# Performance work log

Measured on AMD Instinct MI355X. Metric: run time of the kernel, lower is better.

## Reference

```python
import jax, jax.numpy as jnp
import numpy as np

B, C, T = 8, 1025, 3000


def setup_inputs() -> dict:
    key = jax.random.key(0)
    k1, k2 = jax.random.split(key)
    x_real = jax.random.normal(k1, (B, C, T), dtype=jnp.float32)
    x_imag = jax.random.normal(k2, (B, C, T), dtype=jnp.float32)
    return {"x_real": x_real, "x_imag": x_imag}


def reference(x_real, x_imag):
    # coherent_polar: magnitude + min-max-normalized unwrapped phase, cat on channel dim
    magnitude = jnp.sqrt(x_real * x_real + x_imag * x_imag)  # torch.abs(complex)
    phase = jnp.arctan2(x_imag, x_real)                      # torch.angle

    pi = jnp.float32(np.pi)
    two_pi = jnp.float32(2.0 * np.pi)

    phase_diff = phase[:, :, 1:] - phase[:, :, :-1]          # [B, C, T-1]
    # per-step correction: +2pi where diff < -pi, -2pi where diff > pi
    steps = jnp.where(phase_diff < -pi, two_pi, jnp.float32(0.0)) \
          + jnp.where(phase_diff > pi, -two_pi, jnp.float32(0.0))
    # the original sequential loop is an inclusive prefix-sum of the steps
    correction = jnp.concatenate(
        [jnp.zeros_like(phase[:, :, :1]), jnp.cumsum(steps, axis=2)], axis=2
    )  # [B, C, T]

    unwrapped = phase + correction
    phase_min = jnp.min(unwrapped, axis=2, keepdims=True)
    phase_max = jnp.max(unwrapped, axis=2, keepdims=True)
    phase_norm = (unwrapped - phase_min) / (phase_max - phase_min + 1e-8)

    return jnp.concatenate([magnitude, phase_norm], axis=1)  # [B, 2C, T]
```

## Files before the change

### kernel.cpp

```cpp
#include <hip/hip_runtime.h>

namespace {
constexpr int kB = 8;
constexpr int kC = 1025;
constexpr int kRows = kB * kC;
constexpr int kT = 3000;
constexpr int kThreads = 256;
constexpr int kWaves = kThreads / 64;
constexpr int kSeg = kThreads * 4;
constexpr int kNSeg = 3;
constexpr int kGridB = 2050;
constexpr int kRowsPer = 4;
constexpr float kPi = 3.14159265358979323846f;
constexpr float kTwoPi = 6.28318530717958647692f;
constexpr float kPiO2 = 1.57079632679489661923f;
}

typedef float v4f __attribute__((ext_vector_type(4)));
typedef float v2f __attribute__((ext_vector_type(2)));

__device__ __forceinline__ void sync_lds() {
  asm volatile("s_waitcnt lgkmcnt(0)" ::: "memory");
  __builtin_amdgcn_s_barrier();
  asm volatile("" ::: "memory");
}

__device__ __forceinline__ v2f atan_core2(v2f t) {
  const v2f s = t * t;
  v2f p = v2f{0.00282363896258175373f, 0.00282363896258175373f};
  p = p * s + v2f{-0.0159569028764963150f, -0.0159569028764963150f};
  p = p * s + v2f{0.0425049886107444763f, 0.0425049886107444763f};
  p = p * s + v2f{-0.0748900920152664185f, -0.0748900920152664185f};
  p = p * s + v2f{0.106347933411598206f, 0.106347933411598206f};
  p = p * s + v2f{-0.142027363181114197f, -0.142027363181114197f};
  p = p * s + v2f{0.199926957488059998f, 0.199926957488059998f};
  p = p * s + v2f{-0.333331018686294556f, -0.333331018686294556f};
  return (p * s) * t + t;
}

__device__ __forceinline__ void fast_atan2_4(const v4f y4, const v4f x4,
                                             float out[4]) {
  float t[4], ax[4], ay[4];
  const float xs[4] = {x4.x, x4.y, x4.z, x4.w};
  const float ys[4] = {y4.x, y4.y, y4.z, y4.w};
#pragma unroll
  for (int k = 0; k < 4; ++k) {
    ax[k] = __builtin_fabsf(xs[k]);
    ay[k] = __builtin_fabsf(ys[k]);
    const float mx = fmaxf(ax[k], ay[k]);
    const float mn = fminf(ax[k], ay[k]);
    float tt = mn * __builtin_amdgcn_rcpf(mx);
    if (mx == 0.0f) tt = 0.0f;
    t[k] = tt;
  }
  const v2f a01 = atan_core2(v2f{t[0], t[1]});
  const v2f a23 = atan_core2(v2f{t[2], t[3]});
  const float av[4] = {a01.x, a01.y, a23.x, a23.y};
#pragma unroll
  for (int k = 0; k < 4; ++k) {
    float a = av[k];
    a = (ay[k] > ax[k]) ? (kPiO2 - a) : a;
    a = (xs[k] < 0.0f) ? (kPi - a) : a;
    out[k] = copysignf(a, ys[k]);
  }
}

__device__ __forceinline__ void load_row(const float* __restrict__ re,
                                         const float* __restrict__ im,
                                         int tid, v4f r4[kNSeg], v4f i4[kNSeg]) {
#pragma unroll
  for (int s = 0; s < kNSeg; ++s) {
    const int off = s * kSeg + tid * 4;
    if (s < 2 || off < kT) {
      r4[s] = *reinterpret_cast<const v4f*>(re + off);
      i4[s] = *reinterpret_cast<const v4f*>(im + off);
    }
  }
}

__global__ __launch_bounds__(kThreads, 4) void coherent_polar_kernel(
    const float* __restrict__ xr, const float* __restrict__ xi,
    float* __restrict__ out) {
  __shared__ float s_last[kNSeg][kThreads];
  __shared__ float s_wsum[kWaves][kNSeg];
  __shared__ float s_wmin[kWaves][kNSeg];
  __shared__ float s_wmax[kWaves][kNSeg];

  const int bid = blockIdx.x;
  const int tid = threadIdx.x;
  const int lane = tid & 63;
  const int wave = tid >> 6;
  const bool act2 = tid * 4 + 2 * kSeg < kT;

  v4f r4[kNSeg], i4[kNSeg], r4n[kNSeg], i4n[kNSeg];
  load_row(xr + (size_t)bid * kT, xi + (size_t)bid * kT, tid, r4, i4);

#pragma unroll 1
  for (int r = 0; r < kRowsPer; ++r) {
    const int row = bid + r * kGridB;
    const int b = row / kC;
    const int c = row - b * kC;
    float* mag_out = out + ((size_t)b * (2 * kC) + c) * kT;
    float* ph_out  = out + ((size_t)b * (2 * kC) + kC + c) * kT;

    float ph[kNSeg][4];
#pragma unroll
    for (int s = 0; s < kNSeg; ++s) {
      if (s < 2 || act2) {
        v4f m4;
        m4.x = __builtin_amdgcn_sqrtf(fmaf(r4[s].x, r4[s].x, i4[s].x * i4[s].x));
        m4.y = __builtin_amdgcn_sqrtf(fmaf(r4[s].y, r4[s].y, i4[s].y * i4[s].y));
        m4.z = __builtin_amdgcn_sqrtf(fmaf(r4[s].z, r4[s].z, i4[s].z * i4[s].z));
        m4.w = __builtin_amdgcn_sqrtf(fmaf(r4[s].w, r4[s].w, i4[s].w * i4[s].w));
        __builtin_nontemporal_store(m4, reinterpret_cast<v4f*>(mag_out + s * kSeg + tid * 4));
        fast_atan2_4(i4[s], r4[s], ph[s]);
      }
    }

    if (r + 1 < kRowsPer) {
      const int nrow = row + kGridB;
      load_row(xr + (size_t)nrow * kT, xi + (size_t)nrow * kT, tid, r4n, i4n);
    }

#pragma unroll
    for (int s = 0; s < kNSeg; ++s)
      s_last[s][tid] = (s < 2 || act2) ? ph[s][3] : 0.0f;
    sync_lds();
    float prevph[kNSeg];
#pragma unroll
    for (int s = 0; s < kNSeg; ++s) {
      if (tid > 0)       prevph[s] = s_last[s][tid - 1];
      else if (s > 0)    prevph[s] = s_last[s - 1][kThreads - 1];
      else               prevph[s] = ph[0][0];
    }

    float T[kNSeg];
#pragma unroll
    for (int s = 0; s < kNSeg; ++s) {
      float run = 0.0f;
      if (s < 2 || act2) {
        float p = prevph[s];
#pragma unroll
        for (int k = 0; k < 4; ++k) {
          const float cur = ph[s][k];
          const float d = cur - p;
          p = cur;
          float step = 0.0f;
          if (d < -kPi) step = kTwoPi;
          else if (d > kPi) step = -kTwoPi;
          run += step;
          ph[s][k] = cur + run;
        }
      }
      T[s] = (s < 2 || act2) ? run : 0.0f;
    }

    float inc[kNSeg] = {T[0], T[1], T[2]};
#pragma unroll
    for (int d = 1; d < 64; d <<= 1) {
#pragma unroll
      for (int s = 0; s < kNSeg; ++s) {
        const float n = __shfl_up(inc[s], d);
        if (lane >= d) inc[s] += n;
      }
    }
    float excl[kNSeg];
#pragma unroll
    for (int s = 0; s < kNSeg; ++s) excl[s] = inc[s] - T[s];

    float mn[kNSeg], mx[kNSeg];
#pragma unroll
    for (int s = 0; s < kNSeg; ++s) {
      mn[s] = __builtin_inff();
      mx[s] = -__builtin_inff();
      if (s < 2 || act2) {
#pragma unroll
        for (int k = 0; k < 4; ++k) {
          const float u = ph[s][k] + excl[s];
          mn[s] = fminf(mn[s], u);
          mx[s] = fmaxf(mx[s], u);
        }
      }
    }
#pragma unroll
    for (int m = 32; m >= 1; m >>= 1) {
#pragma unroll
      for (int s = 0; s < kNSeg; ++s) {
        mn[s] = fminf(mn[s], __shfl_xor(mn[s], m));
        mx[s] = fmaxf(mx[s], __shfl_xor(mx[s], m));
      }
    }
    if (lane == 63) {
#pragma unroll
      for (int s = 0; s < kNSeg; ++s) s_wsum[wave][s] = inc[s];
    }
    if (lane == 0) {
#pragma unroll
      for (int s = 0; s < kNSeg; ++s) { s_wmin[wave][s] = mn[s]; s_wmax[wave][s] = mx[s]; }
    }
    sync_lds();

    float wavePref[kWaves][kNSeg];
    float blockTot[kNSeg];
#pragma unroll
    for (int s = 0; s < kNSeg; ++s) {
      float acc = 0.0f;
#pragma unroll
      for (int w = 0; w < kWaves; ++w) { wavePref[w][s] = acc; acc += s_wsum[w][s]; }
      blockTot[s] = acc;
    }
    float segBase[kNSeg];
    segBase[0] = 0.0f;
    segBase[1] = blockTot[0];
    segBase[2] = blockTot[0] + blockTot[1];

    float gmn = __builtin_inff();
    float gmx = -__builtin_inff();
#pragma unroll
    for (int w = 0; w < kWaves; ++w) {
#pragma unroll
      for (int s = 0; s < kNSeg; ++s) {
        const float off = segBase[s] + wavePref[w][s];
        gmn = fminf(gmn, s_wmin[w][s] + off);
        gmx = fmaxf(gmx, s_wmax[w][s] + off);
      }
    }
    const float inv = 1.0f / (gmx - gmn + 1e-8f);

#pragma unroll
    for (int s = 0; s < kNSeg; ++s) {
      if (s < 2 || act2) {
        const float base = segBase[s] + wavePref[wave][s] + excl[s] - gmn;
        v4f o;
        o.x = (ph[s][0] + base) * inv;
        o.y = (ph[s][1] + base) * inv;
        o.z = (ph[s][2] + base) * inv;
        o.w = (ph[s][3] + base) * inv;
        __builtin_nontemporal_store(o, reinterpret_cast<v4f*>(ph_out + s * kSeg + tid * 4));
      }
    }

    if (r + 1 < kRowsPer) {
#pragma unroll
      for (int s = 0; s < kNSeg; ++s) { r4[s] = r4n[s]; i4[s] = i4n[s]; }
    }
  }
}

extern "C" void kernel_launch(void* const* d_in, const int* in_sizes, int n_in,
                              void* d_out, int out_size, void* d_ws, size_t ws_size,
                              hipStream_t stream) {
  const float* xr = (const float*)d_in[0];
  const float* xi = (const float*)d_in[1];
  float* out = (float*)d_out;
  coherent_polar_kernel<<<dim3(kGridB), dim3(kThreads), 0, stream>>>(xr, xi, out);
}
```

Measured before the change: 70.18 us.

## Give each wave a contiguous segment and cut block scan to one barrier

Each wave now owns a contiguous 768-element chunk of the row, so the inter-thread phase boundary is handled with shuffles and readlane instead of an LDS exchange and barrier. Wrap counts are packed as three 10-bit integers into one word, giving a single integer shuffle scan instead of three float scans. The min/max reduction uses DPP row operations, and cross-wave combination uses a double-buffered LDS slot with one barrier per row. The next-row prefetch is also issued before compute. This relies on the packed counts not overflowing their 10-bit fields, and it adds register pressure from the early prefetch.

```diff
diff --git a/kernel.cpp b/kernel.cpp
--- a/kernel.cpp
+++ b/kernel.cpp
@@ -3,17 +3,17 @@
 namespace {
 constexpr int kB = 8;
 constexpr int kC = 1025;
-constexpr int kRows = kB * kC;
 constexpr int kT = 3000;
 constexpr int kThreads = 256;
-constexpr int kWaves = kThreads / 64;
-constexpr int kSeg = kThreads * 4;
-constexpr int kNSeg = 3;
+constexpr int kWSeg = 768;
+constexpr int kSub = 256;
+constexpr int kNS = 3;
 constexpr int kGridB = 2050;
 constexpr int kRowsPer = 4;
 constexpr float kPi = 3.14159265358979323846f;
 constexpr float kTwoPi = 6.28318530717958647692f;
 constexpr float kPiO2 = 1.57079632679489661923f;
+constexpr float kInv2Pi = 0.15915494309189533577f;
 }
 
 typedef float v4f __attribute__((ext_vector_type(4)));
@@ -23,6 +23,28 @@
   asm volatile("s_waitcnt lgkmcnt(0)" ::: "memory");
   __builtin_amdgcn_s_barrier();
   asm volatile("" ::: "memory");
+}
+
+__device__ __forceinline__ float rdlane_f(float v, int l) {
+  return __builtin_bit_cast(
+      float, __builtin_amdgcn_readlane(__builtin_bit_cast(int, v), l));
+}
+
+template <int kCtrl>
+__device__ __forceinline__ float dpp_f(float v) {
+  return __builtin_bit_cast(
+      float, __builtin_amdgcn_update_dpp(__builtin_bit_cast(int, v),
+                                         __builtin_bit_cast(int, v), kCtrl,
+                                         0xF, 0xF, false));
+}
+
+__device__ __forceinline__ void wave_minmax63(float& mn, float& mx) {
+  mn = fminf(mn, dpp_f<0x121>(mn)); mx = fmaxf(mx, dpp_f<0x121>(mx));
+  mn = fminf(mn, dpp_f<0x122>(mn)); mx = fmaxf(mx, dpp_f<0x122>(mx));
+  mn = fminf(mn, dpp_f<0x124>(mn)); mx = fmaxf(mx, dpp_f<0x124>(mx));
+  mn = fminf(mn, dpp_f<0x128>(mn)); mx = fmaxf(mx, dpp_f<0x128>(mx));
+  mn = fminf(mn, dpp_f<0x142>(mn)); mx = fmaxf(mx, dpp_f<0x142>(mx));
+  mn = fminf(mn, dpp_f<0x143>(mn)); mx = fmaxf(mx, dpp_f<0x143>(mx));
 }
 
 __device__ __forceinline__ v2f atan_core2(v2f t) {
@@ -65,35 +87,37 @@
   }
 }
 
-__device__ __forceinline__ void load_row(const float* __restrict__ re,
-                                         const float* __restrict__ im,
-                                         int tid, v4f r4[kNSeg], v4f i4[kNSeg]) {
-#pragma unroll
-  for (int s = 0; s < kNSeg; ++s) {
-    const int off = s * kSeg + tid * 4;
-    if (s < 2 || off < kT) {
-      r4[s] = *reinterpret_cast<const v4f*>(re + off);
-      i4[s] = *reinterpret_cast<const v4f*>(im + off);
-    }
-  }
-}
-
 __global__ __launch_bounds__(kThreads, 4) void coherent_polar_kernel(
     const float* __restrict__ xr, const float* __restrict__ xi,
     float* __restrict__ out) {
-  __shared__ float s_last[kNSeg][kThreads];
-  __shared__ float s_wsum[kWaves][kNSeg];
-  __shared__ float s_wmin[kWaves][kNSeg];
-  __shared__ float s_wmax[kWaves][kNSeg];
+  __shared__ __align__(16) float s_comb[2][5][4];
 
   const int bid = blockIdx.x;
   const int tid = threadIdx.x;
   const int lane = tid & 63;
   const int wave = tid >> 6;
-  const bool act2 = tid * 4 + 2 * kSeg < kT;
-
-  v4f r4[kNSeg], i4[kNSeg], r4n[kNSeg], i4n[kNSeg];
-  load_row(xr + (size_t)bid * kT, xi + (size_t)bid * kT, tid, r4, i4);
+
+  int offs[kNS];
+  bool act[kNS];
+#pragma unroll
+  for (int s = 0; s < kNS; ++s) {
+    offs[s] = wave * kWSeg + s * kSub + lane * 4;
+    act[s] = offs[s] < kT;
+  }
+  const int tail_lane = (wave == 3) ? 45 : 63;
+
+  v4f r4[kNS], i4[kNS], r4n[kNS], i4n[kNS];
+  {
+    const float* re = xr + (size_t)bid * kT;
+    const float* im = xi + (size_t)bid * kT;
+#pragma unroll
+    for (int s = 0; s < kNS; ++s) {
+      if (act[s]) {
+        r4[s] = *reinterpret_cast<const v4f*>(re + offs[s]);
+        i4[s] = *reinterpret_cast<const v4f*>(im + offs[s]);
+      }
+    }
+  }
 
 #pragma unroll 1
   for (int r = 0; r < kRowsPer; ++r) {
@@ -102,44 +126,55 @@
     const int c = row - b * kC;
     float* mag_out = out + ((size_t)b * (2 * kC) + c) * kT;
     float* ph_out  = out + ((size_t)b * (2 * kC) + kC + c) * kT;
-
-    float ph[kNSeg][4];
-#pragma unroll
-    for (int s = 0; s < kNSeg; ++s) {
-      if (s < 2 || act2) {
+    const int par = r & 1;
+
+    if (r + 1 < kRowsPer) {
+      const int nrow = row + kGridB;
+      const float* re = xr + (size_t)nrow * kT;
+      const float* im = xi + (size_t)nrow * kT;
+#pragma unroll
+      for (int s = 0; s < kNS; ++s) {
+        if (act[s]) {
+          r4n[s] = *reinterpret_cast<const v4f*>(re + offs[s]);
+          i4n[s] = *reinterpret_cast<const v4f*>(im + offs[s]);
+        }
+      }
+    }
+
+    float ph[kNS][4];
+#pragma unroll
+    for (int s = 0; s < kNS; ++s) {
+      if (act[s]) {
         v4f m4;
         m4.x = __builtin_amdgcn_sqrtf(fmaf(r4[s].x, r4[s].x, i4[s].x * i4[s].x));
         m4.y = __builtin_amdgcn_sqrtf(fmaf(r4[s].y, r4[s].y, i4[s].y * i4[s].y));
         m4.z = __builtin_amdgcn_sqrtf(fmaf(r4[s].z, r4[s].z, i4[s].z * i4[s].z));
         m4.w = __builtin_amdgcn_sqrtf(fmaf(r4[s].w, r4[s].w, i4[s].w * i4[s].w));
-        __builtin_nontemporal_store(m4, reinterpret_cast<v4f*>(mag_out + s * kSeg + tid * 4));
+        __builtin_nontemporal_store(m4, reinterpret_cast<v4f*>(mag_out + offs[s]));
         fast_atan2_4(i4[s], r4[s], ph[s]);
       }
     }
 
-    if (r + 1 < kRowsPer) {
-      const int nrow = row + kGridB;
-      load_row(xr + (size_t)nrow * kT, xi + (size_t)nrow * kT, tid, r4n, i4n);
-    }
-
-#pragma unroll
-    for (int s = 0; s < kNSeg; ++s)
-      s_last[s][tid] = (s < 2 || act2) ? ph[s][3] : 0.0f;
-    sync_lds();
-    float prevph[kNSeg];
-#pragma unroll
-    for (int s = 0; s < kNSeg; ++s) {
-      if (tid > 0)       prevph[s] = s_last[s][tid - 1];
-      else if (s > 0)    prevph[s] = s_last[s - 1][kThreads - 1];
-      else               prevph[s] = ph[0][0];
-    }
-
-    float T[kNSeg];
-#pragma unroll
-    for (int s = 0; s < kNSeg; ++s) {
+    const float rawhead = ph[0][0];
+    float rawtail[kNS];
+#pragma unroll
+    for (int s = 0; s < kNS; ++s) rawtail[s] = ph[s][3];
+
+    float prev[kNS];
+#pragma unroll
+    for (int s = 0; s < kNS; ++s) {
+      float pv = __shfl_up(rawtail[s], 1);
+      if (lane == 0)
+        pv = (s == 0) ? rawhead : rdlane_f(rawtail[s - 1], 63);
+      prev[s] = pv;
+    }
+
+    int n[kNS];
+#pragma unroll
+    for (int s = 0; s < kNS; ++s) {
       float run = 0.0f;
-      if (s < 2 || act2) {
-        float p = prevph[s];
+      if (act[s]) {
+        float p = prev[s];
 #pragma unroll
         for (int k = 0; k < 4; ++k) {
           const float cur = ph[s][k];
@@ -152,97 +187,107 @@
           ph[s][k] = cur + run;
         }
       }
-      T[s] = (s < 2 || act2) ? run : 0.0f;
-    }
-
-    float inc[kNSeg] = {T[0], T[1], T[2]};
+      n[s] = __float2int_rn(run * kInv2Pi);
+    }
+
+    const unsigned packed = (unsigned)(n[0] + 8) |
+                            ((unsigned)(n[1] + 8) << 10) |
+                            ((unsigned)(n[2] + 8) << 20);
+    unsigned incp = packed;
 #pragma unroll
     for (int d = 1; d < 64; d <<= 1) {
-#pragma unroll
-      for (int s = 0; s < kNSeg; ++s) {
-        const float n = __shfl_up(inc[s], d);
-        if (lane >= d) inc[s] += n;
-      }
-    }
-    float excl[kNSeg];
-#pragma unroll
-    for (int s = 0; s < kNSeg; ++s) excl[s] = inc[s] - T[s];
-
-    float mn[kNSeg], mx[kNSeg];
-#pragma unroll
-    for (int s = 0; s < kNSeg; ++s) {
-      mn[s] = __builtin_inff();
-      mx[s] = -__builtin_inff();
-      if (s < 2 || act2) {
+      const unsigned up = (unsigned)__shfl_up((int)incp, d);
+      if (lane >= d) incp += up;
+    }
+    const unsigned excp = incp - packed;
+    const unsigned i63 = (unsigned)__builtin_amdgcn_readlane((int)incp, 63);
+    const int tot0 = (int)(i63 & 1023u) - 512;
+    const int tot1 = (int)((i63 >> 10) & 1023u) - 512;
+    const int tot2 = (int)((i63 >> 20) & 1023u) - 512;
+    int cnt[kNS];
+    cnt[0] = (int)(excp & 1023u) - 8 * lane;
+    cnt[1] = (int)((excp >> 10) & 1023u) - 8 * lane + tot0;
+    cnt[2] = (int)((excp >> 20) & 1023u) - 8 * lane + tot0 + tot1;
+
+    float mn = __builtin_inff();
+    float mx = -__builtin_inff();
+    float woff[kNS];
+#pragma unroll
+    for (int s = 0; s < kNS; ++s) {
+      woff[s] = (float)cnt[s] * kTwoPi;
+      if (act[s]) {
 #pragma unroll
         for (int k = 0; k < 4; ++k) {
-          const float u = ph[s][k] + excl[s];
-          mn[s] = fminf(mn[s], u);
-          mx[s] = fmaxf(mx[s], u);
+          const float u = ph[s][k] + woff[s];
+          mn = fminf(mn, u);
+          mx = fmaxf(mx, u);
         }
       }
     }
-#pragma unroll
-    for (int m = 32; m >= 1; m >>= 1) {
-#pragma unroll
-      for (int s = 0; s < kNSeg; ++s) {
-        mn[s] = fminf(mn[s], __shfl_xor(mn[s], m));
-        mx[s] = fmaxf(mx[s], __shfl_xor(mx[s], m));
-      }
-    }
+    wave_minmax63(mn, mx);
+
+    const float tailv = rdlane_f(rawtail[2], tail_lane);
+    const float headv = rdlane_f(rawhead, 0);
     if (lane == 63) {
-#pragma unroll
-      for (int s = 0; s < kNSeg; ++s) s_wsum[wave][s] = inc[s];
-    }
-    if (lane == 0) {
-#pragma unroll
-      for (int s = 0; s < kNSeg; ++s) { s_wmin[wave][s] = mn[s]; s_wmax[wave][s] = mx[s]; }
+      s_comb[par][0][wave] = headv;
+      s_comb[par][1][wave] = tailv;
+      s_comb[par][2][wave] = (float)(tot0 + tot1 + tot2);
+      s_comb[par][3][wave] = mn;
+      s_comb[par][4][wave] = mx;
     }
     sync_lds();
 
-    float wavePref[kWaves][kNSeg];
-    float blockTot[kNSeg];
-#pragma unroll
-    for (int s = 0; s < kNSeg; ++s) {
-      float acc = 0.0f;
-#pragma unroll
-      for (int w = 0; w < kWaves; ++w) { wavePref[w][s] = acc; acc += s_wsum[w][s]; }
-      blockTot[s] = acc;
-    }
-    float segBase[kNSeg];
-    segBase[0] = 0.0f;
-    segBase[1] = blockTot[0];
-    segBase[2] = blockTot[0] + blockTot[1];
-
+    const v4f hd = *reinterpret_cast<const v4f*>(&s_comb[par][0][0]);
+    const v4f tl = *reinterpret_cast<const v4f*>(&s_comb[par][1][0]);
+    const v4f tw = *reinterpret_cast<const v4f*>(&s_comb[par][2][0]);
+    const v4f wm = *reinterpret_cast<const v4f*>(&s_comb[par][3][0]);
+    const v4f wx = *reinterpret_cast<const v4f*>(&s_comb[par][4][0]);
+
+    float C[4];
+    C[0] = 0.0f;
+    {
+      float cum = 0.0f;
+      const float hds[4] = {hd.x, hd.y, hd.z, hd.w};
+      const float tls[4] = {tl.x, tl.y, tl.z, tl.w};
+      const float tws[4] = {tw.x, tw.y, tw.z, tw.w};
+#pragma unroll
+      for (int w = 1; w < 4; ++w) {
+        const float d = hds[w] - tls[w - 1];
+        float nb = 0.0f;
+        if (d < -kPi) nb = 1.0f;
+        else if (d > kPi) nb = -1.0f;
+        cum += tws[w - 1] + nb;
+        C[w] = cum;
+      }
+    }
+    const float wms[4] = {wm.x, wm.y, wm.z, wm.w};
+    const float wxs[4] = {wx.x, wx.y, wx.z, wx.w};
     float gmn = __builtin_inff();
     float gmx = -__builtin_inff();
 #pragma unroll
-    for (int w = 0; w < kWaves; ++w) {
-#pragma unroll
-      for (int s = 0; s < kNSeg; ++s) {
-        const float off = segBase[s] + wavePref[w][s];
-        gmn = fminf(gmn, s_wmin[w][s] + off);
-        gmx = fmaxf(gmx, s_wmax[w][s] + off);
-      }
+    for (int w = 0; w < 4; ++w) {
+      gmn = fminf(gmn, wms[w] + C[w] * kTwoPi);
+      gmx = fmaxf(gmx, wxs[w] + C[w] * kTwoPi);
     }
     const float inv = 1.0f / (gmx - gmn + 1e-8f);
-
-#pragma unroll
-    for (int s = 0; s < kNSeg; ++s) {
-      if (s < 2 || act2) {
-        const float base = segBase[s] + wavePref[wave][s] + excl[s] - gmn;
+    const float myC = C[wave] * kTwoPi;
+
+#pragma unroll
+    for (int s = 0; s < kNS; ++s) {
+      if (act[s]) {
+        const float base = myC + woff[s] - gmn;
         v4f o;
         o.x = (ph[s][0] + base) * inv;
         o.y = (ph[s][1] + base) * inv;
         o.z = (ph[s][2] + base) * inv;
         o.w = (ph[s][3] + base) * inv;
-        __builtin_nontemporal_store(o, reinterpret_cast<v4f*>(ph_out + s * kSeg + tid * 4));
+        __builtin_nontemporal_store(o, reinterpret_cast<v4f*>(ph_out + offs[s]));
       }
     }
 
     if (r + 1 < kRowsPer) {
 #pragma unroll
-      for (int s = 0; s < kNSeg; ++s) { r4[s] = r4n[s]; i4[s] = i4n[s]; }
+      for (int s = 0; s < kNS; ++s) { r4[s] = r4n[s]; i4[s] = i4n[s]; }
     }
   }
 }
```

Result: no change. 69.83 us (-0.5%).
